# Kernel tuning notes

Hardware: AMD Instinct MI355X
Metric: run time of the kernel (lower is better)

Reference implementation:

```python
import jax, jax.numpy as jnp
import numpy as np

B, T, V, Dw, Df, H, L, F_ = 16, 96, 32000, 512, 512, 1024, 100, 64
EPS = 1e-8
SOS = 0


def setup_inputs() -> dict:
    key = jax.random.key(0)
    ks = jax.random.split(key, 24)
    rn = lambda k, s, sc=0.02: (jax.random.normal(k, s) * sc).astype(jnp.float32)
    pos_mask = (jax.random.uniform(ks[1], (B, F_, L)) < 0.3).astype(jnp.float32)
    pos_mask = jnp.maximum(pos_mask, jax.nn.one_hot(jnp.zeros((B, F_), jnp.int32), L))
    return {
        "fact_embeddings": rn(ks[0], (B, F_, Df), 1.0),
        "pos_mask": pos_mask,
        "emb": rn(ks[2], (V, Dw), 0.05),
        "W_ih": rn(ks[3], (4 * H, Df + Dw + L)),
        "W_hh": rn(ks[4], (4 * H, H)),
        "b_ih": jnp.zeros(4 * H, jnp.float32),
        "b_hh": jnp.zeros(4 * H, jnp.float32),
        "Wf1": rn(ks[5], (H, H + Df)), "bf1": jnp.zeros(H, jnp.float32),
        "Wf2": rn(ks[6], (Df, H)), "bf2": jnp.zeros(Df, jnp.float32),
        "Wc1": rn(ks[7], (H, H + Df)), "bc1": jnp.zeros(H, jnp.float32),
        "Wc2": rn(ks[8], (1, H)), "bc2": jnp.zeros(1, jnp.float32),
        "Wv1": rn(ks[9], (H, H + Df)), "bv1": jnp.zeros(H, jnp.float32),
        "Wv2": rn(ks[10], (Dw, H)), "bv2": jnp.zeros(Dw, jnp.float32),
        "Wp1": rn(ks[11], (H, H + Df)), "bp1": jnp.zeros(H, jnp.float32),
        "Wp2": rn(ks[12], (100, H)), "bp2": jnp.zeros(100, jnp.float32),
        "WP": rn(ks[13], (L, 100)), "bP": jnp.zeros(L, jnp.float32),
        "true_w": jax.random.randint(ks[14], (B, T), 0, L),
        "true_a": jax.random.randint(ks[15], (B, T), 0, F_),
        "true_z": jax.random.randint(ks[16], (B, T), 0, 2),
        "num_facts": jax.random.randint(ks[17], (B,), 1, F_),
    }


def reference(fact_embeddings, pos_mask, emb, W_ih, W_hh, b_ih, b_hh,
              Wf1, bf1, Wf2, bf2, Wc1, bc1, Wc2, bc2,
              Wv1, bv1, Wv2, bv2, Wp1, bp1, Wp2, bp2, WP, bP,
              true_w, true_a, true_z, num_facts):
    def mlp(x, W1, b1, W2, b2):
        return W2 @ jax.nn.relu(W1 @ x + b1) + b2

    def single(fe, pmask_b, tw, ta, tz, nf):
        # fe: [F_, Df]  pmask_b: [F_, L]  tw/ta/tz: [T]
        idx = jnp.arange(F_)
        valid = (idx < nf).astype(jnp.float32)
        attn_mask = jnp.where(idx == F_ - 1, 1.0, valid)  # NaF slot always allowed
        e_k = (fe * valid[:, None]).sum(0) / nf.astype(jnp.float32)

        def step(carry, inputs):
            a_prev, h, c, wv, wo = carry
            w_t, a_true, z_true = inputs
            x = jnp.concatenate([a_prev, wv, wo])  # [Df+Dw+L]
            gates = W_ih @ x + b_ih + W_hh @ h + b_hh
            i_g, f_g, g_g, o_g = jnp.split(gates, 4)
            c = jax.nn.sigmoid(f_g) * c + jax.nn.sigmoid(i_g) * jnp.tanh(g_g)
            h = jax.nn.sigmoid(o_g) * jnp.tanh(c)
            oe = jnp.concatenate([h, e_k])
            k_fact = mlp(oe, Wf1, bf1, Wf2, bf2)           # [Df]
            prob_a = jax.nn.softmax(fe @ k_fact)           # [F_]
            m = attn_mask * prob_a + EPS
            m = m / m.sum()
            log_m = jnp.log(m)
            a_idx = jnp.argmax(m)
            a_vec = fe[a_idx]
            oa = jnp.concatenate([h, a_vec])
            z = jax.nn.sigmoid(mlp(oa, Wc1, bc1, Wc2, bc2))[0]
            k_voca = mlp(oa, Wv1, bv1, Wv2, bv2)           # [Dw]
            log_w = jax.nn.log_softmax(emb @ k_voca)       # [V]
            k_pos = mlp(oa, Wp1, bp1, Wp2, bp2)            # [100]
            prob_pos = jax.nn.softmax(WP @ k_pos + bP)     # [L]
            mp = pmask_b[a_true] * prob_pos + EPS
            mp = mp / mp.sum()
            log_pos = jnp.log(mp)
            zf = z_true.astype(jnp.float32)
            loss = (-log_m[a_true]
                    + jnp.where(z_true == 0, -log_w[w_t], -log_pos[w_t])
                    - (zf * jnp.log(z) + (1.0 - zf) * jnp.log(1.0 - z)))
            wv_next = jnp.where(z_true == 0, emb[w_t], jnp.zeros(Dw, jnp.float32))
            wo_next = jnp.where(z_true == 0, jnp.zeros(L, jnp.float32), jax.nn.one_hot(w_t, L))
            return (a_vec, h, c, wv_next, wo_next), loss

        carry0 = (jnp.zeros(Df, jnp.float32), jnp.zeros(H, jnp.float32),
                  jnp.zeros(H, jnp.float32), emb[SOS], jnp.zeros(L, jnp.float32))
        _, losses = jax.lax.scan(step, carry0, (tw, ta, tz))
        return losses.sum()

    return jax.vmap(single)(fact_embeddings, pos_mask, true_w, true_a, true_z, num_facts).sum()
```

## Files before the change

kernel.cpp:

```cpp
#include <hip/hip_runtime.h>
#include <math.h>

#define TT 96
#define VV 32000
#define EPSF 1e-8f

typedef __attribute__((ext_vector_type(8))) short short8;
typedef __attribute__((ext_vector_type(4))) float f4v;

__device__ __forceinline__ float wsum64(float v){
  #pragma unroll
  for (int m=32;m>0;m>>=1) v += __shfl_xor(v,m);
  return v;
}
__device__ __forceinline__ float sigm(float x){ return 1.0f/(1.0f+expf(-x)); }
__device__ __forceinline__ float softplus(float x){ return x>20.0f ? x : log1pf(expf(x)); }
__device__ __forceinline__ float bf2f(unsigned short u){ return __uint_as_float(((unsigned)u)<<16); }
__device__ __forceinline__ unsigned short f2bf(float f){
  unsigned u = __float_as_uint(f);
  return (unsigned short)((u + 0x7fffu + ((u>>16)&1u)) >> 16);
}

__device__ __forceinline__ void core_chunk(
  const float4* __restrict__ w0, const float4* __restrict__ w1,
  const float4* __restrict__ w2, const float4* __restrict__ w3,
  const float4* __restrict__ xl, int l, int g, float (&acc)[4][4])
{
  #pragma unroll
  for (int kt=0; kt<8; kt++){
    int i = kt*16 + l;
    float4 a0=w0[i], a1=w1[i], a2=w2[i], a3=w3[i];
    #pragma unroll
    for (int j=0;j<4;j++){
      float4 x = xl[(4*g+j)*129 + i];
      acc[0][j] += a0.x*x.x + a0.y*x.y + a0.z*x.z + a0.w*x.w;
      acc[1][j] += a1.x*x.x + a1.y*x.y + a1.z*x.z + a1.w*x.w;
      acc[2][j] += a2.x*x.x + a2.y*x.y + a2.z*x.z + a2.w*x.w;
      acc[3][j] += a3.x*x.x + a3.y*x.y + a3.z*x.z + a3.w*x.w;
    }
  }
}

__device__ __forceinline__ float reduce_pick(float (&acc)[4][4], int l){
  float r = 0.f;
  #pragma unroll
  for (int ri=0;ri<4;ri++)
  #pragma unroll
  for (int j=0;j<4;j++){
    float v = acc[ri][j];
    v += __shfl_xor(v,1); v += __shfl_xor(v,2);
    v += __shfl_xor(v,4); v += __shfl_xor(v,8);
    if (l == ri*4+j) r = v;
  }
  return r;
}


__global__ __launch_bounds__(256) void k_step1(
  const float* __restrict__ Whh, float* __restrict__ hall,
  const float* __restrict__ Pw, const float* __restrict__ Pa,
  const int* __restrict__ aall, float* __restrict__ c, int t)
{
  __shared__ float4 xl[16*129];
  __shared__ float sg[256];
  int tid = threadIdx.x, lane = tid & 63, wave = tid >> 6;
  int l = lane & 15, g = lane >> 4;
  int j0 = blockIdx.x*4;
  const float4* h4 = (const float4*)hall + (size_t)t*4096;
  float acc[4][4] = {};
  for (int kc=0; kc<2; kc++){
    for (int idx=tid; idx<2048; idx+=256){
      int b = idx>>7, i = idx&127;
      xl[b*129+i] = h4[b*256 + kc*128 + i];
    }
    __syncthreads();
    const float4* w0 = (const float4*)(Whh + (size_t)(wave*1024 + j0+0)*1024) + kc*128;
    const float4* w1 = (const float4*)(Whh + (size_t)(wave*1024 + j0+1)*1024) + kc*128;
    const float4* w2 = (const float4*)(Whh + (size_t)(wave*1024 + j0+2)*1024) + kc*128;
    const float4* w3 = (const float4*)(Whh + (size_t)(wave*1024 + j0+3)*1024) + kc*128;
    core_chunk(w0,w1,w2,w3, xl, l, g, acc);
    __syncthreads();
  }
  float v = reduce_pick(acc, l);
  int r = l>>2;
  int b = g*4 + (l&3);
  int row = wave*1024 + j0 + r;
  float e = Pw[((size_t)(b*96+t))*4096 + row];
  if (t > 0){
    int ai = aall[(t-1)*16 + b];
    e += Pa[((size_t)(b*64+ai))*4096 + row];
  }
  sg[wave*64 + r*16 + b] = v + e;
  __syncthreads();
  if (tid < 64){
    int jj = j0 + (tid>>4), bb = tid&15;
    float ig = sg[  0 + (tid>>4)*16 + bb];
    float fg = sg[ 64 + (tid>>4)*16 + bb];
    float gg = sg[128 + (tid>>4)*16 + bb];
    float og = sg[192 + (tid>>4)*16 + bb];
    int ci = bb*1024 + jj;
    float cn = sigm(fg)*c[ci] + sigm(ig)*tanhf(gg);
    c[ci] = cn;
    hall[((size_t)(t+1)*16 + bb)*1024 + jj] = sigm(og)*tanhf(cn);
  }
}

__global__ __launch_bounds__(256) void k_tf(
  const float* __restrict__ Wf1, const float* __restrict__ hall,
  const float* __restrict__ cf, float* __restrict__ tf, int t)
{
  __shared__ float4 xl[16*129];
  int tid = threadIdx.x, lane = tid & 63, wave = tid >> 6;
  int l = lane & 15, g = lane >> 4;
  int rl0 = blockIdx.x*16 + wave*4;
  const float4* h4 = (const float4*)hall + (size_t)(t+1)*4096;
  float acc[4][4] = {};
  for (int kc=0; kc<2; kc++){
    for (int idx=tid; idx<2048; idx+=256){
      int b = idx>>7, i = idx&127;
      xl[b*129+i] = h4[b*256 + kc*128 + i];
    }
    __syncthreads();
    const float4* w0 = (const float4*)(Wf1 + (size_t)(rl0+0)*1536) + kc*128;
    const float4* w1 = (const float4*)(Wf1 + (size_t)(rl0+1)*1536) + kc*128;
    const float4* w2 = (const float4*)(Wf1 + (size_t)(rl0+2)*1536) + kc*128;
    const float4* w3 = (const float4*)(Wf1 + (size_t)(rl0+3)*1536) + kc*128;
    core_chunk(w0,w1,w2,w3, xl, l, g, acc);
    __syncthreads();
  }
  float v = reduce_pick(acc, l);
  int rl = rl0 + (l>>2);
  int b = g*4 + (l&3);
  tf[b*1024 + rl] = fmaxf(v + cf[b*1024 + rl], 0.f);
}

__global__ __launch_bounds__(256) void k_fk(
  const float* __restrict__ Wf2, const float* __restrict__ bf2,
  const float* __restrict__ tf, float* __restrict__ kfact)
{
  __shared__ float4 xl[16*129];
  int tid = threadIdx.x, lane = tid & 63, wave = tid >> 6;
  int l = lane & 15, g = lane >> 4;
  int row0 = blockIdx.x*16 + wave*4;
  const float4* X4 = (const float4*)tf;
  float acc[4][4] = {};
  for (int kc=0; kc<2; kc++){
    for (int idx=tid; idx<2048; idx+=256){
      int b = idx>>7, i = idx&127;
      xl[b*129+i] = X4[b*256 + kc*128 + i];
    }
    __syncthreads();
    const float4* w0 = (const float4*)(Wf2 + (size_t)(row0+0)*1024) + kc*128;
    const float4* w1 = (const float4*)(Wf2 + (size_t)(row0+1)*1024) + kc*128;
    const float4* w2 = (const float4*)(Wf2 + (size_t)(row0+2)*1024) + kc*128;
    const float4* w3 = (const float4*)(Wf2 + (size_t)(row0+3)*1024) + kc*128;
    core_chunk(w0,w1,w2,w3, xl, l, g, acc);
    __syncthreads();
  }
  float v = reduce_pick(acc, l);
  int row = row0 + (l>>2);
  int b = g*4 + (l&3);
  kfact[b*512 + row] = v + bf2[row];
}

__global__ __launch_bounds__(256) void k_attn(
  const float* __restrict__ fe, const float* __restrict__ kfact,
  const int* __restrict__ ta, const int* __restrict__ nfp,
  int* __restrict__ aall, float* __restrict__ loss, int t)
{
  __shared__ float sS[64];
  int b = blockIdx.x, tid = threadIdx.x;
  int f = tid >> 2, q = tid & 3;
  const float4* fe4 = (const float4*)(fe + ((size_t)b*64 + f)*512);
  const float4* kf4 = (const float4*)(kfact + b*512);
  float acc = 0.f;
  for (int j=0;j<32;j++){
    int i = q*32 + j;
    float4 a = fe4[i], k = kf4[i];
    acc += a.x*k.x + a.y*k.y + a.z*k.z + a.w*k.w;
  }
  acc += __shfl_xor(acc,1);
  acc += __shfl_xor(acc,2);
  if (q==0) sS[f] = acc;
  __syncthreads();
  if (tid < 64){
    int nf = nfp[b];
    float s = sS[tid];
    float mx = s;
    #pragma unroll
    for (int m=32;m>0;m>>=1) mx = fmaxf(mx, __shfl_xor(mx,m));
    float p = expf(s - mx);
    float ps = wsum64(p);
    p /= ps;
    bool mask = (tid < nf) || (tid == 63);
    float mval = mask ? (p + EPSF) : EPSF;
    float msum = wsum64(mval);
    float bv = mval; int bi2 = tid;
    #pragma unroll
    for (int m=32;m>0;m>>=1){
      float ov = __shfl_xor(bv,m); int oi = __shfl_xor(bi2,m);
      if (ov > bv || (ov == bv && oi < bi2)){ bv = ov; bi2 = oi; }
    }
    int at = ta[b*TT + t];
    float mat = __shfl(mval, at);
    if (tid == 0){
      atomicAdd(loss, -(logf(mat) - logf(msum)));
      aall[t*16 + b] = bi2;
    }
  }
}


__global__ __launch_bounds__(256) void k2_cvp(
  const float* __restrict__ Wc1, const float* __restrict__ Wv1,
  const float* __restrict__ Wp1, const float* __restrict__ hall,
  const float* __restrict__ Ph, const int* __restrict__ aall,
  const float* __restrict__ bc1, const float* __restrict__ bv1,
  const float* __restrict__ bp1, float* __restrict__ tcvp)
{
  __shared__ float4 xl[16*129];
  int tid = threadIdx.x, lane = tid & 63, wave = tid >> 6;
  int l = lane & 15, g = lane >> 4;
  int seg = blockIdx.x >> 6;
  int rl0 = (blockIdx.x & 63)*16 + wave*4;
  const float* W = (seg==0)?Wc1:(seg==1)?Wv1:Wp1;
  const float4* h4 = (const float4*)hall + (size_t)(16 + blockIdx.y*16)*256;
  float acc[4][4] = {};
  for (int kc=0; kc<2; kc++){
    for (int idx=tid; idx<2048; idx+=256){
      int cc = idx>>7, i = idx&127;
      xl[cc*129+i] = h4[cc*256 + kc*128 + i];
    }
    __syncthreads();
    const float4* w0 = (const float4*)(W + (size_t)(rl0+0)*1536) + kc*128;
    const float4* w1 = (const float4*)(W + (size_t)(rl0+1)*1536) + kc*128;
    const float4* w2 = (const float4*)(W + (size_t)(rl0+2)*1536) + kc*128;
    const float4* w3 = (const float4*)(W + (size_t)(rl0+3)*1536) + kc*128;
    core_chunk(w0,w1,w2,w3, xl, l, g, acc);
    __syncthreads();
  }
  float v = reduce_pick(acc, l);
  int rl = rl0 + (l>>2);
  int n = blockIdx.y*16 + g*4 + (l&3);
  int b = n & 15;
  int ai = aall[n];
  const float* bias = (seg==0)?bc1:(seg==1)?bv1:bp1;
  float vv = v + Ph[((size_t)(b*64+ai))*3072 + seg*1024 + rl] + bias[rl];
  tcvp[(size_t)n*3072 + seg*1024 + rl] = fmaxf(vv, 0.f);
}

__global__ __launch_bounds__(256) void k2_heads2(
  const float* __restrict__ Wv2, const float* __restrict__ bv2,
  const float* __restrict__ Wp2, const float* __restrict__ bp2,
  const float* __restrict__ Wc2, const float* __restrict__ bc2,
  const float* __restrict__ tcvp, unsigned short* __restrict__ kvh,
  float* __restrict__ kpall, float* __restrict__ zlall)
{
  __shared__ float4 xl[16*129];
  int tid = threadIdx.x, lane = tid & 63, wave = tid >> 6;
  int l = lane & 15, g = lane >> 4;
  int bx = blockIdx.x;
  int seg = (bx < 32) ? 0 : (bx < 39) ? 1 : 2;
  int rb  = (seg==0) ? bx*16 : (seg==1) ? (bx-32)*16 : 0;
  int rl0 = rb + wave*4;
  const float* WS = (seg==0)?Wv2:(seg==1)?Wp2:Wc2;
  int maxr = (seg==0)?511:(seg==1)?99:0;
  int xoff4 = (seg==0)?256:(seg==1)?512:0;
  const float4* X4 = (const float4*)tcvp;
  float acc[4][4] = {};
  for (int kc=0; kc<2; kc++){
    for (int idx=tid; idx<2048; idx+=256){
      int cc = idx>>7, i = idx&127;
      xl[cc*129+i] = X4[(size_t)(blockIdx.y*16+cc)*768 + xoff4 + kc*128 + i];
    }
    __syncthreads();
    const float4* w0 = (const float4*)(WS + (size_t)min(rl0+0,maxr)*1024) + kc*128;
    const float4* w1 = (const float4*)(WS + (size_t)min(rl0+1,maxr)*1024) + kc*128;
    const float4* w2 = (const float4*)(WS + (size_t)min(rl0+2,maxr)*1024) + kc*128;
    const float4* w3 = (const float4*)(WS + (size_t)min(rl0+3,maxr)*1024) + kc*128;
    core_chunk(w0,w1,w2,w3, xl, l, g, acc);
    __syncthreads();
  }
  float v = reduce_pick(acc, l);
  int rl = rl0 + (l>>2);
  int n = blockIdx.y*16 + g*4 + (l&3);
  if (seg==0) kvh[(size_t)n*512 + rl] = f2bf(v + bv2[rl]);
  else if (seg==1){ if (rl < 100) kpall[n*128 + rl] = v + bp2[rl]; }
  else { if (rl == 0) zlall[n] = v + bc2[0]; }
}

__global__ __launch_bounds__(256) void k2_vocab(
  const unsigned short* __restrict__ embh, const unsigned short* __restrict__ kvh,
  float2* __restrict__ part)
{
  int wid = blockIdx.x*4 + (threadIdx.x>>6);
  int lane = threadIdx.x & 63;
  int mtile = wid % 500, ntile = wid / 500;
  int mrow = mtile*64 + (lane&15);
  int ncol = ntile*64 + (lane&15);
  int ko = (lane>>4)*8;
  f4v acc[4][4];
  #pragma unroll
  for (int i=0;i<4;i++)
  #pragma unroll
  for (int j=0;j<4;j++)
  #pragma unroll
  for (int r=0;r<4;r++) acc[i][j][r] = 0.f;
  for (int kk=0; kk<512; kk+=32){
    short8 af[4], bfr[4];
    #pragma unroll
    for (int i=0;i<4;i++)
      af[i] = *(const short8*)(embh + (size_t)(mrow+16*i)*512 + kk + ko);
    #pragma unroll
    for (int i=0;i<4;i++)
      bfr[i] = *(const short8*)(kvh + (size_t)(ncol+16*i)*512 + kk + ko);
    #pragma unroll
    for (int i=0;i<4;i++)
      #pragma unroll
      for (int j=0;j<4;j++)
        acc[i][j] = __builtin_amdgcn_mfma_f32_16x16x32_bf16(af[i], bfr[j], acc[i][j], 0,0,0);
  }
  int q = lane>>4;
  #pragma unroll
  for (int j=0;j<4;j++){
    float mx = -3.4e38f;
    #pragma unroll
    for (int i=0;i<4;i++)
    #pragma unroll
    for (int r=0;r<4;r++) mx = fmaxf(mx, acc[i][j][r]);
    mx = fmaxf(mx, __shfl_xor(mx,16));
    mx = fmaxf(mx, __shfl_xor(mx,32));
    float s = 0.f;
    #pragma unroll
    for (int i=0;i<4;i++)
    #pragma unroll
    for (int r=0;r<4;r++) s += expf(acc[i][j][r] - mx);
    s += __shfl_xor(s,16);
    s += __shfl_xor(s,32);
    if (q==0){
      int col = ntile*64 + 16*j + (lane&15);
      part[(size_t)col*500 + mtile] = make_float2(mx, s);
    }
  }
}

__global__ __launch_bounds__(256) void k2_vfin(
  const float2* __restrict__ part, const unsigned short* __restrict__ embh,
  const unsigned short* __restrict__ kvh, const int* __restrict__ tw,
  const int* __restrict__ tz, float* __restrict__ loss)
{
  __shared__ float red[4];
  int n = blockIdx.x, tid = threadIdx.x;
  int t = n>>4, b = n&15;
  float mx = -3.4e38f;
  for (int i=tid; i<500; i+=256) mx = fmaxf(mx, part[(size_t)n*500+i].x);
  #pragma unroll
  for (int m=32;m>0;m>>=1) mx = fmaxf(mx, __shfl_xor(mx,m));
  if ((tid&63)==0) red[tid>>6] = mx;
  __syncthreads();
  float M = fmaxf(fmaxf(red[0],red[1]), fmaxf(red[2],red[3]));
  __syncthreads();
  float s = 0.f;
  for (int i=tid; i<500; i+=256){
    float2 p = part[(size_t)n*500+i];
    s += p.y * expf(p.x - M);
  }
  s = wsum64(s);
  if ((tid&63)==0) red[tid>>6] = s;
  __syncthreads();
  float S = red[0]+red[1]+red[2]+red[3];
  __syncthreads();
  int w = tw[b*96+t];
  float d = 0.f;
  {
    const unsigned short* er = embh + (size_t)w*512;
    const unsigned short* kr = kvh + (size_t)n*512;
    for (int i=tid; i<512; i+=256) d += bf2f(er[i])*bf2f(kr[i]);
  }
  d = wsum64(d);
  if ((tid&63)==0) red[tid>>6] = d;
  __syncthreads();
  if (tid==0 && tz[b*96+t]==0){
    float D = red[0]+red[1]+red[2]+red[3];
    atomicAdd(loss, -(D - (M + logf(S))));
  }
}

__global__ __launch_bounds__(128) void k2_posz(
  const float* __restrict__ kpall, const float* __restrict__ zlall,
  const float* __restrict__ WP, const float* __restrict__ bP,
  const float* __restrict__ pmask, const int* __restrict__ tw,
  const int* __restrict__ ta, const int* __restrict__ tz,
  float* __restrict__ loss)
{
  __shared__ float pp[100];
  int n = blockIdx.x, tid = threadIdx.x;
  int t = n>>4, b = n&15;
  if (tid < 100){
    float s = bP[tid];
    const float* wr = WP + tid*100;
    const float* kp = kpall + n*128;
    for (int j=0;j<100;j++) s += wr[j]*kp[j];
    pp[tid] = s;
  }
  __syncthreads();
  if (tid == 0){
    float u = zlall[n];
    int z = tz[b*96+t], w = tw[b*96+t], at = ta[b*96+t];
    float tot = z ? softplus(-u) : softplus(u);
    if (z){
      float mxv = -1e30f;
      for (int l2=0;l2<100;l2++) mxv = fmaxf(mxv, pp[l2]);
      float se = 0.f;
      for (int l2=0;l2<100;l2++) se += expf(pp[l2]-mxv);
      const float* pm = pmask + ((size_t)b*64 + at)*100;
      float msum = 0.f, mw = 0.f;
      for (int l2=0;l2<100;l2++){
        float m = pm[l2]*(expf(pp[l2]-mxv)/se) + EPSF;
        msum += m;
        if (l2==w) mw = m;
      }
      tot += -(logf(mw) - logf(msum));
    }
    atomicAdd(loss, tot);
  }
}


__global__ void k_cvt_emb(const float* __restrict__ emb, unsigned* __restrict__ out){
  const int n = VV*512/2;
  for (int idx = blockIdx.x*256 + threadIdx.x; idx < n; idx += gridDim.x*256){
    float2 v = ((const float2*)emb)[idx];
    unsigned a = __float_as_uint(v.x), b = __float_as_uint(v.y);
    unsigned ra = (a + 0x7fffu + ((a>>16)&1u)) >> 16;
    unsigned rb = (b + 0x7fffu + ((b>>16)&1u)) >> 16;
    out[idx] = ra | (rb<<16);
  }
}

__global__ void k_setup(const float* __restrict__ fe, const int* __restrict__ nfp,
                        float* __restrict__ e_k){
  int b = blockIdx.x, tid = threadIdx.x;
  int nf = nfp[b];
  for (int d=tid; d<512; d+=256){
    float s = 0.f;
    for (int f=0; f<nf; f++) s += fe[((size_t)b*64+f)*512 + d];
    e_k[b*512+d] = s/(float)nf;
  }
}

__global__ __launch_bounds__(256) void k_pre_pa(
  const float* __restrict__ Wih, const float* __restrict__ fe, float* __restrict__ Pa)
{
  __shared__ float4 xl[16*129];
  int tid = threadIdx.x, lane = tid & 63, wave = tid >> 6;
  int l = lane & 15, g = lane >> 4;
  int row0 = blockIdx.x*16 + wave*4;
  int c0 = blockIdx.y*16;
  const float4* fe4 = (const float4*)fe;
  for (int idx=tid; idx<2048; idx+=256){
    int cc = idx>>7, i = idx&127;
    xl[cc*129+i] = fe4[(size_t)(c0+cc)*128 + i];
  }
  __syncthreads();
  const float4* w0 = (const float4*)(Wih + (size_t)(row0+0)*1124);
  const float4* w1 = (const float4*)(Wih + (size_t)(row0+1)*1124);
  const float4* w2 = (const float4*)(Wih + (size_t)(row0+2)*1124);
  const float4* w3 = (const float4*)(Wih + (size_t)(row0+3)*1124);
  float acc[4][4] = {};
  core_chunk(w0,w1,w2,w3, xl, l, g, acc);
  float v = reduce_pick(acc, l);
  int row = row0 + (l>>2), c = c0 + g*4 + (l&3);
  Pa[(size_t)c*4096 + row] = v;
}

__global__ __launch_bounds__(256) void k_pre_ph(
  const float* __restrict__ Wc1, const float* __restrict__ Wv1,
  const float* __restrict__ Wp1, const float* __restrict__ fe, float* __restrict__ Ph)
{
  __shared__ float4 xl[16*129];
  int tid = threadIdx.x, lane = tid & 63, wave = tid >> 6;
  int l = lane & 15, g = lane >> 4;
  int row0 = blockIdx.x*16 + wave*4;
  int head = row0 >> 10, rl0 = row0 & 1023;
  const float* W = (head==0)?Wc1:(head==1)?Wv1:Wp1;
  int c0 = blockIdx.y*16;
  const float4* fe4 = (const float4*)fe;
  for (int idx=tid; idx<2048; idx+=256){
    int cc = idx>>7, i = idx&127;
    xl[cc*129+i] = fe4[(size_t)(c0+cc)*128 + i];
  }
  __syncthreads();
  const float4* w0 = (const float4*)(W + (size_t)(rl0+0)*1536 + 1024);
  const float4* w1 = (const float4*)(W + (size_t)(rl0+1)*1536 + 1024);
  const float4* w2 = (const float4*)(W + (size_t)(rl0+2)*1536 + 1024);
  const float4* w3 = (const float4*)(W + (size_t)(rl0+3)*1536 + 1024);
  float acc[4][4] = {};
  core_chunk(w0,w1,w2,w3, xl, l, g, acc);
  float v = reduce_pick(acc, l);
  int row = row0 + (l>>2), c = c0 + g*4 + (l&3);
  Ph[(size_t)c*3072 + row] = v;
}

__global__ __launch_bounds__(256) void k_pre_pw(
  const float* __restrict__ Wih, const float* __restrict__ emb,
  const int* __restrict__ tw, const int* __restrict__ tz,
  const float* __restrict__ bih, const float* __restrict__ bhh,
  float* __restrict__ Pw)
{
  __shared__ float4 xl[16*129];
  int tid = threadIdx.x, lane = tid & 63, wave = tid >> 6;
  int l = lane & 15, g = lane >> 4;
  int row0 = blockIdx.x*16 + wave*4;
  int c0 = blockIdx.y*16;
  for (int idx=tid; idx<2048; idx+=256){
    int cc = idx>>7, i = idx&127;
    int c = c0+cc, b = c/96, t2 = c - b*96;
    int w=0, z=0;
    if (t2>0){ w = tw[b*96+t2-1]; z = tz[b*96+t2-1]; }
    float4 v = make_float4(0.f,0.f,0.f,0.f);
    if (z==0) v = ((const float4*)emb)[(size_t)w*128 + i];
    xl[cc*129+i] = v;
  }
  __syncthreads();
  const float4* w0 = (const float4*)(Wih + (size_t)(row0+0)*1124 + 512);
  const float4* w1 = (const float4*)(Wih + (size_t)(row0+1)*1124 + 512);
  const float4* w2 = (const float4*)(Wih + (size_t)(row0+2)*1124 + 512);
  const float4* w3 = (const float4*)(Wih + (size_t)(row0+3)*1124 + 512);
  float acc[4][4] = {};
  core_chunk(w0,w1,w2,w3, xl, l, g, acc);
  float v = reduce_pick(acc, l);
  int row = row0 + (l>>2), c = c0 + g*4 + (l&3);
  int b = c/96, t2 = c - b*96;
  int w=0, z=0;
  if (t2>0){ w = tw[b*96+t2-1]; z = tz[b*96+t2-1]; }
  v += bih[row] + bhh[row];
  if (z) v += Wih[(size_t)row*1124 + 1024 + w];
  Pw[(size_t)c*4096 + row] = v;
}

__global__ __launch_bounds__(256) void k_pre_cf(
  const float* __restrict__ Wf1, const float* __restrict__ bf1,
  const float* __restrict__ e_k, float* __restrict__ cf)
{
  __shared__ float4 xl[16*129];
  int tid = threadIdx.x, lane = tid & 63, wave = tid >> 6;
  int l = lane & 15, g = lane >> 4;
  int row0 = blockIdx.x*16 + wave*4;
  const float4* ek4 = (const float4*)e_k;
  for (int idx=tid; idx<2048; idx+=256){
    int cc = idx>>7, i = idx&127;
    xl[cc*129+i] = ek4[cc*128 + i];
  }
  __syncthreads();
  const float4* w0 = (const float4*)(Wf1 + (size_t)(row0+0)*1536 + 1024);
  const float4* w1 = (const float4*)(Wf1 + (size_t)(row0+1)*1536 + 1024);
  const float4* w2 = (const float4*)(Wf1 + (size_t)(row0+2)*1536 + 1024);
  const float4* w3 = (const float4*)(Wf1 + (size_t)(row0+3)*1536 + 1024);
  float acc[4][4] = {};
  core_chunk(w0,w1,w2,w3, xl, l, g, acc);
  float v = reduce_pick(acc, l);
  int row = row0 + (l>>2), b = g*4 + (l&3);
  cf[b*1024 + row] = v + bf1[row];
}

__global__ void k_out(const float* __restrict__ loss, float* __restrict__ out){
  out[0] = loss[0];
}

extern "C" void kernel_launch(void* const* d_in, const int* in_sizes, int n_in,
                              void* d_out, int out_size, void* d_ws, size_t ws_size,
                              hipStream_t stream)
{
  const float* fe   = (const float*)d_in[0];
  const float* pmask= (const float*)d_in[1];
  const float* emb  = (const float*)d_in[2];
  const float* Wih  = (const float*)d_in[3];
  const float* Whh  = (const float*)d_in[4];
  const float* bih  = (const float*)d_in[5];
  const float* bhh  = (const float*)d_in[6];
  const float* Wf1  = (const float*)d_in[7];
  const float* bf1  = (const float*)d_in[8];
  const float* Wf2  = (const float*)d_in[9];
  const float* bf2  = (const float*)d_in[10];
  const float* Wc1  = (const float*)d_in[11];
  const float* bc1  = (const float*)d_in[12];
  const float* Wc2  = (const float*)d_in[13];
  const float* bc2  = (const float*)d_in[14];
  const float* Wv1  = (const float*)d_in[15];
  const float* bv1  = (const float*)d_in[16];
  const float* Wv2  = (const float*)d_in[17];
  const float* bv2  = (const float*)d_in[18];
  const float* Wp1  = (const float*)d_in[19];
  const float* bp1  = (const float*)d_in[20];
  const float* Wp2  = (const float*)d_in[21];
  const float* bp2  = (const float*)d_in[22];
  const float* WP   = (const float*)d_in[23];
  const float* bP   = (const float*)d_in[24];
  const int* tw  = (const int*)d_in[25];
  const int* ta  = (const int*)d_in[26];
  const int* tz  = (const int*)d_in[27];
  const int* nfp = (const int*)d_in[28];

  float* w = (float*)d_ws;
  float*    loss  = w + 0;
  float*    c     = w + 16;
  float*    hall  = w + 16400;
  int*      aall  = (int*)(w + 1605648);
  float*    tf    = w + 1607184;
  float*    kfact = w + 1623568;
  float*    e_k   = w + 1631760;
  float*    cf    = w + 1639952;
  float*    kpall = w + 1656336;
  float*    zlall = w + 1852944;
  float*    tcvp  = w + 1854480;
  float2*   part  = (float2*)(w + 6573072);
  unsigned short* kvh = (unsigned short*)(w + 8109072);
  float*    Pa    = w + 8502288;
  float*    Ph    = w + 12696592;
  float*    Pw    = w + 15842320;
  unsigned* embbf = (unsigned*)(w + 22133776);
  const unsigned short* embh = (const unsigned short*)embbf;

  hipMemsetAsync(d_ws, 0, (size_t)(16 + 16384 + 16384)*4, stream);
  k_cvt_emb<<<8192,256,0,stream>>>(emb, embbf);
  k_setup<<<16,256,0,stream>>>(fe, nfp, e_k);
  k_pre_pa<<<dim3(256,64),256,0,stream>>>(Wih, fe, Pa);
  k_pre_ph<<<dim3(192,64),256,0,stream>>>(Wc1, Wv1, Wp1, fe, Ph);
  k_pre_pw<<<dim3(256,96),256,0,stream>>>(Wih, emb, tw, tz, bih, bhh, Pw);
  k_pre_cf<<<64,256,0,stream>>>(Wf1, bf1, e_k, cf);

  for (int t=0; t<TT; t++){
    k_step1<<<256,256,0,stream>>>(Whh, hall, Pw, Pa, aall, c, t);
    k_tf<<<64,256,0,stream>>>(Wf1, hall, cf, tf, t);
    k_fk<<<32,256,0,stream>>>(Wf2, bf2, tf, kfact);
    k_attn<<<16,256,0,stream>>>(fe, kfact, ta, nfp, aall, loss, t);
  }

  k2_cvp<<<dim3(192,96),256,0,stream>>>(Wc1, Wv1, Wp1, hall, Ph, aall,
                                        bc1, bv1, bp1, tcvp);
  k2_heads2<<<dim3(40,96),256,0,stream>>>(Wv2, bv2, Wp2, bp2, Wc2, bc2,
                                          tcvp, kvh, kpall, zlall);
  k2_vocab<<<3000,256,0,stream>>>(embh, kvh, part);
  k2_vfin<<<1536,256,0,stream>>>(part, embh, kvh, tw, tz, loss);
  k2_posz<<<1536,128,0,stream>>>(kpall, zlall, WP, bP, pmask, tw, ta, tz, loss);
  k_out<<<1,1,0,stream>>>(loss, (float*)d_out);
}
```

Baseline: 5.350 ms.

## Fuse recurrent loop into persistent kernel with grid barriers and fold Wf2

The per-timestep launches of four small kernels are replaced by one persistent 256-block kernel. It loops over all timesteps and separates the LSTM, the fact-MLP hidden layer and the attention stages with a global atomic-counter barrier. The second fact-MLP layer is folded algebraically into a precomputed fact_embeddings·Wf2 product (Gb) plus a bias term, which removes a dependent matmul stage per step. This targets launch overhead and serial stage latency. In exchange it relies on all 256 blocks being co-resident, adds spin-wait barrier costs, and makes the attention dot products longer (1024 instead of 512).

Measured after the change: 15.34 ms. +186.7%, slower.

```diff
diff --git a/kernel.cpp b/kernel.cpp
--- a/kernel.cpp
+++ b/kernel.cpp
@@ -21,6 +21,19 @@
   return (unsigned short)((u + 0x7fffu + ((u>>16)&1u)) >> 16);
 }
 
+__device__ __forceinline__ void gbar(unsigned* cnt, unsigned target){
+  __syncthreads();
+  if (threadIdx.x == 0){
+    __threadfence();
+    __hip_atomic_fetch_add(cnt, 1u, __ATOMIC_ACQ_REL, __HIP_MEMORY_SCOPE_AGENT);
+    while (__hip_atomic_load(cnt, __ATOMIC_ACQUIRE, __HIP_MEMORY_SCOPE_AGENT) < target){
+      __builtin_amdgcn_s_sleep(1);
+    }
+    __threadfence();
+  }
+  __syncthreads();
+}
+
 __device__ __forceinline__ void core_chunk(
   const float4* __restrict__ w0, const float4* __restrict__ w1,
   const float4* __restrict__ w2, const float4* __restrict__ w3,
@@ -55,158 +68,137 @@
   return r;
 }
 
-
-__global__ __launch_bounds__(256) void k_step1(
+__global__ __launch_bounds__(256) void k_phase1(
   const float* __restrict__ Whh, float* __restrict__ hall,
   const float* __restrict__ Pw, const float* __restrict__ Pa,
-  const int* __restrict__ aall, float* __restrict__ c, int t)
+  int* __restrict__ aall, float* __restrict__ c,
+  const float* __restrict__ Wf1, const float* __restrict__ cf,
+  float* __restrict__ tf,
+  const float* __restrict__ Gb, const float* __restrict__ gb0,
+  const int* __restrict__ ta, const int* __restrict__ nfp,
+  float* __restrict__ loss, unsigned* __restrict__ bar)
 {
   __shared__ float4 xl[16*129];
   __shared__ float sg[256];
+  __shared__ float sS[64];
   int tid = threadIdx.x, lane = tid & 63, wave = tid >> 6;
   int l = lane & 15, g = lane >> 4;
-  int j0 = blockIdx.x*4;
-  const float4* h4 = (const float4*)hall + (size_t)t*4096;
-  float acc[4][4] = {};
-  for (int kc=0; kc<2; kc++){
-    for (int idx=tid; idx<2048; idx+=256){
-      int b = idx>>7, i = idx&127;
-      xl[b*129+i] = h4[b*256 + kc*128 + i];
-    }
-    __syncthreads();
-    const float4* w0 = (const float4*)(Whh + (size_t)(wave*1024 + j0+0)*1024) + kc*128;
-    const float4* w1 = (const float4*)(Whh + (size_t)(wave*1024 + j0+1)*1024) + kc*128;
-    const float4* w2 = (const float4*)(Whh + (size_t)(wave*1024 + j0+2)*1024) + kc*128;
-    const float4* w3 = (const float4*)(Whh + (size_t)(wave*1024 + j0+3)*1024) + kc*128;
-    core_chunk(w0,w1,w2,w3, xl, l, g, acc);
-    __syncthreads();
-  }
-  float v = reduce_pick(acc, l);
-  int r = l>>2;
-  int b = g*4 + (l&3);
-  int row = wave*1024 + j0 + r;
-  float e = Pw[((size_t)(b*96+t))*4096 + row];
-  if (t > 0){
-    int ai = aall[(t-1)*16 + b];
-    e += Pa[((size_t)(b*64+ai))*4096 + row];
-  }
-  sg[wave*64 + r*16 + b] = v + e;
-  __syncthreads();
-  if (tid < 64){
-    int jj = j0 + (tid>>4), bb = tid&15;
-    float ig = sg[  0 + (tid>>4)*16 + bb];
-    float fg = sg[ 64 + (tid>>4)*16 + bb];
-    float gg = sg[128 + (tid>>4)*16 + bb];
-    float og = sg[192 + (tid>>4)*16 + bb];
-    int ci = bb*1024 + jj;
-    float cn = sigm(fg)*c[ci] + sigm(ig)*tanhf(gg);
-    c[ci] = cn;
-    hall[((size_t)(t+1)*16 + bb)*1024 + jj] = sigm(og)*tanhf(cn);
-  }
-}
-
-__global__ __launch_bounds__(256) void k_tf(
-  const float* __restrict__ Wf1, const float* __restrict__ hall,
-  const float* __restrict__ cf, float* __restrict__ tf, int t)
-{
-  __shared__ float4 xl[16*129];
-  int tid = threadIdx.x, lane = tid & 63, wave = tid >> 6;
-  int l = lane & 15, g = lane >> 4;
-  int rl0 = blockIdx.x*16 + wave*4;
-  const float4* h4 = (const float4*)hall + (size_t)(t+1)*4096;
-  float acc[4][4] = {};
-  for (int kc=0; kc<2; kc++){
-    for (int idx=tid; idx<2048; idx+=256){
-      int b = idx>>7, i = idx&127;
-      xl[b*129+i] = h4[b*256 + kc*128 + i];
-    }
-    __syncthreads();
-    const float4* w0 = (const float4*)(Wf1 + (size_t)(rl0+0)*1536) + kc*128;
-    const float4* w1 = (const float4*)(Wf1 + (size_t)(rl0+1)*1536) + kc*128;
-    const float4* w2 = (const float4*)(Wf1 + (size_t)(rl0+2)*1536) + kc*128;
-    const float4* w3 = (const float4*)(Wf1 + (size_t)(rl0+3)*1536) + kc*128;
-    core_chunk(w0,w1,w2,w3, xl, l, g, acc);
-    __syncthreads();
-  }
-  float v = reduce_pick(acc, l);
-  int rl = rl0 + (l>>2);
-  int b = g*4 + (l&3);
-  tf[b*1024 + rl] = fmaxf(v + cf[b*1024 + rl], 0.f);
-}
-
-__global__ __launch_bounds__(256) void k_fk(
-  const float* __restrict__ Wf2, const float* __restrict__ bf2,
-  const float* __restrict__ tf, float* __restrict__ kfact)
-{
-  __shared__ float4 xl[16*129];
-  int tid = threadIdx.x, lane = tid & 63, wave = tid >> 6;
-  int l = lane & 15, g = lane >> 4;
-  int row0 = blockIdx.x*16 + wave*4;
-  const float4* X4 = (const float4*)tf;
-  float acc[4][4] = {};
-  for (int kc=0; kc<2; kc++){
-    for (int idx=tid; idx<2048; idx+=256){
-      int b = idx>>7, i = idx&127;
-      xl[b*129+i] = X4[b*256 + kc*128 + i];
-    }
-    __syncthreads();
-    const float4* w0 = (const float4*)(Wf2 + (size_t)(row0+0)*1024) + kc*128;
-    const float4* w1 = (const float4*)(Wf2 + (size_t)(row0+1)*1024) + kc*128;
-    const float4* w2 = (const float4*)(Wf2 + (size_t)(row0+2)*1024) + kc*128;
-    const float4* w3 = (const float4*)(Wf2 + (size_t)(row0+3)*1024) + kc*128;
-    core_chunk(w0,w1,w2,w3, xl, l, g, acc);
-    __syncthreads();
-  }
-  float v = reduce_pick(acc, l);
-  int row = row0 + (l>>2);
-  int b = g*4 + (l&3);
-  kfact[b*512 + row] = v + bf2[row];
-}
-
-__global__ __launch_bounds__(256) void k_attn(
-  const float* __restrict__ fe, const float* __restrict__ kfact,
-  const int* __restrict__ ta, const int* __restrict__ nfp,
-  int* __restrict__ aall, float* __restrict__ loss, int t)
-{
-  __shared__ float sS[64];
-  int b = blockIdx.x, tid = threadIdx.x;
-  int f = tid >> 2, q = tid & 3;
-  const float4* fe4 = (const float4*)(fe + ((size_t)b*64 + f)*512);
-  const float4* kf4 = (const float4*)(kfact + b*512);
-  float acc = 0.f;
-  for (int j=0;j<32;j++){
-    int i = q*32 + j;
-    float4 a = fe4[i], k = kf4[i];
-    acc += a.x*k.x + a.y*k.y + a.z*k.z + a.w*k.w;
-  }
-  acc += __shfl_xor(acc,1);
-  acc += __shfl_xor(acc,2);
-  if (q==0) sS[f] = acc;
-  __syncthreads();
-  if (tid < 64){
-    int nf = nfp[b];
-    float s = sS[tid];
-    float mx = s;
-    #pragma unroll
-    for (int m=32;m>0;m>>=1) mx = fmaxf(mx, __shfl_xor(mx,m));
-    float p = expf(s - mx);
-    float ps = wsum64(p);
-    p /= ps;
-    bool mask = (tid < nf) || (tid == 63);
-    float mval = mask ? (p + EPSF) : EPSF;
-    float msum = wsum64(mval);
-    float bv = mval; int bi2 = tid;
-    #pragma unroll
-    for (int m=32;m>0;m>>=1){
-      float ov = __shfl_xor(bv,m); int oi = __shfl_xor(bi2,m);
-      if (ov > bv || (ov == bv && oi < bi2)){ bv = ov; bi2 = oi; }
-    }
-    int at = ta[b*TT + t];
-    float mat = __shfl(mval, at);
-    if (tid == 0){
-      atomicAdd(loss, -(logf(mat) - logf(msum)));
-      aall[t*16 + b] = bi2;
-    }
+  int wg = blockIdx.x;
+  unsigned rnd = 0;
+
+  for (int t=0; t<TT; t++){
+    {
+      int j0 = wg*4;
+      const float4* h4 = (const float4*)hall + (size_t)t*4096;
+      float acc[4][4] = {};
+      for (int kc=0; kc<2; kc++){
+        for (int idx=tid; idx<2048; idx+=256){
+          int b = idx>>7, i = idx&127;
+          xl[b*129+i] = h4[b*256 + kc*128 + i];
+        }
+        __syncthreads();
+        const float4* w0 = (const float4*)(Whh + (size_t)(wave*1024 + j0+0)*1024) + kc*128;
+        const float4* w1 = (const float4*)(Whh + (size_t)(wave*1024 + j0+1)*1024) + kc*128;
+        const float4* w2 = (const float4*)(Whh + (size_t)(wave*1024 + j0+2)*1024) + kc*128;
+        const float4* w3 = (const float4*)(Whh + (size_t)(wave*1024 + j0+3)*1024) + kc*128;
+        core_chunk(w0,w1,w2,w3, xl, l, g, acc);
+        __syncthreads();
+      }
+      float v = reduce_pick(acc, l);
+      int r = l>>2;
+      int b = g*4 + (l&3);
+      int row = wave*1024 + j0 + r;
+      float e = Pw[((size_t)(b*96+t))*4096 + row];
+      if (t > 0){
+        int ai = aall[(t-1)*16 + b];
+        e += Pa[((size_t)(b*64+ai))*4096 + row];
+      }
+      sg[wave*64 + r*16 + b] = v + e;
+      __syncthreads();
+      if (tid < 64){
+        int jj = j0 + (tid>>4), bb = tid&15;
+        float ig = sg[  0 + (tid>>4)*16 + bb];
+        float fg = sg[ 64 + (tid>>4)*16 + bb];
+        float gg = sg[128 + (tid>>4)*16 + bb];
+        float og = sg[192 + (tid>>4)*16 + bb];
+        int ci = bb*1024 + jj;
+        float cn = sigm(fg)*c[ci] + sigm(ig)*tanhf(gg);
+        c[ci] = cn;
+        hall[((size_t)(t+1)*16 + bb)*1024 + jj] = sigm(og)*tanhf(cn);
+      }
+    }
+    rnd++; gbar(bar, rnd*256u);
+
+    if (wg < 64){
+      int rl0 = wg*16 + wave*4;
+      const float4* h4 = (const float4*)hall + (size_t)(t+1)*4096;
+      float acc[4][4] = {};
+      for (int kc=0; kc<2; kc++){
+        for (int idx=tid; idx<2048; idx+=256){
+          int b = idx>>7, i = idx&127;
+          xl[b*129+i] = h4[b*256 + kc*128 + i];
+        }
+        __syncthreads();
+        const float4* w0 = (const float4*)(Wf1 + (size_t)(rl0+0)*1536) + kc*128;
+        const float4* w1 = (const float4*)(Wf1 + (size_t)(rl0+1)*1536) + kc*128;
+        const float4* w2 = (const float4*)(Wf1 + (size_t)(rl0+2)*1536) + kc*128;
+        const float4* w3 = (const float4*)(Wf1 + (size_t)(rl0+3)*1536) + kc*128;
+        core_chunk(w0,w1,w2,w3, xl, l, g, acc);
+        __syncthreads();
+      }
+      float v = reduce_pick(acc, l);
+      int rl = rl0 + (l>>2);
+      int b = g*4 + (l&3);
+      tf[b*1024 + rl] = fmaxf(v + cf[b*1024 + rl], 0.f);
+    }
+    rnd++; gbar(bar, rnd*256u);
+
+    if (wg < 16){
+      int b = wg;
+      float* stf = (float*)xl;
+      ((float4*)stf)[tid] = ((const float4*)(tf + b*1024))[tid];
+      __syncthreads();
+      int f = tid>>2, q = tid&3;
+      const float4* G4 = (const float4*)(Gb + (size_t)(b*64+f)*1024);
+      const float4* st4 = (const float4*)stf;
+      float acc = 0.f;
+      for (int j=0;j<64;j++){
+        int i = q*64 + j;
+        float4 a = G4[i], x = st4[i];
+        acc += a.x*x.x + a.y*x.y + a.z*x.z + a.w*x.w;
+      }
+      acc += __shfl_xor(acc,1);
+      acc += __shfl_xor(acc,2);
+      if (q==0) sS[f] = acc + gb0[b*64+f];
+      __syncthreads();
+      if (tid < 64){
+        int nf = nfp[b];
+        float s = sS[tid];
+        float mx = s;
+        #pragma unroll
+        for (int m=32;m>0;m>>=1) mx = fmaxf(mx, __shfl_xor(mx,m));
+        float p = expf(s - mx);
+        float ps = wsum64(p);
+        p /= ps;
+        bool mask = (tid < nf) || (tid == 63);
+        float mval = mask ? (p + EPSF) : EPSF;
+        float msum = wsum64(mval);
+        float bv = mval; int bi2 = tid;
+        #pragma unroll
+        for (int m=32;m>0;m>>=1){
+          float ov = __shfl_xor(bv,m); int oi = __shfl_xor(bi2,m);
+          if (ov > bv || (ov == bv && oi < bi2)){ bv = ov; bi2 = oi; }
+        }
+        int at = ta[b*TT + t];
+        float mat = __shfl(mval, at);
+        if (tid == 0){
+          atomicAdd(loss, -(logf(mat) - logf(msum)));
+          aall[t*16 + b] = bi2;
+        }
+      }
+      __syncthreads();
+    }
+    rnd++; gbar(bar, rnd*256u);
   }
 }
 
@@ -562,6 +554,49 @@
   float v = reduce_pick(acc, l);
   int row = row0 + (l>>2), b = g*4 + (l&3);
   cf[b*1024 + row] = v + bf1[row];
+}
+
+__global__ __launch_bounds__(256) void k_pre_g(
+  const float* __restrict__ Wf2, const float* __restrict__ fe, float* __restrict__ Gb)
+{
+  __shared__ float fs[16][128];
+  int tid = threadIdx.x;
+  int r0 = blockIdx.x*16;
+  int k0 = blockIdx.y*256;
+  float acc[16] = {};
+  for (int dc=0; dc<4; dc++){
+    for (int idx=tid; idx<2048; idx+=256){
+      int r = idx>>7, d = idx&127;
+      fs[r][d] = fe[(size_t)(r0+r)*512 + dc*128 + d];
+    }
+    __syncthreads();
+    for (int d=0; d<128; d++){
+      float w = Wf2[(size_t)(dc*128+d)*1024 + k0 + tid];
+      #pragma unroll
+      for (int r=0;r<16;r++) acc[r] += fs[r][d]*w;
+    }
+    __syncthreads();
+  }
+  #pragma unroll
+  for (int r=0;r<16;r++) Gb[(size_t)(r0+r)*1024 + k0 + tid] = acc[r];
+}
+
+__global__ __launch_bounds__(256) void k_gb0(
+  const float* __restrict__ fe, const float* __restrict__ bf2, float* __restrict__ gb0)
+{
+  int b = blockIdx.x;
+  int f = threadIdx.x>>2, q = threadIdx.x&3;
+  const float4* fe4 = (const float4*)(fe + ((size_t)b*64+f)*512);
+  const float4* b4 = (const float4*)bf2;
+  float acc = 0.f;
+  for (int j=0;j<32;j++){
+    int i = q*32+j;
+    float4 a = fe4[i], x = b4[i];
+    acc += a.x*x.x + a.y*x.y + a.z*x.z + a.w*x.w;
+  }
+  acc += __shfl_xor(acc,1);
+  acc += __shfl_xor(acc,2);
+  if (q==0) gb0[b*64+f] = acc;
 }
 
 __global__ void k_out(const float* __restrict__ loss, float* __restrict__ out){
@@ -604,16 +639,18 @@
 
   float* w = (float*)d_ws;
   float*    loss  = w + 0;
+  unsigned* bar   = (unsigned*)(w + 8);
   float*    c     = w + 16;
   float*    hall  = w + 16400;
   int*      aall  = (int*)(w + 1605648);
   float*    tf    = w + 1607184;
-  float*    kfact = w + 1623568;
+  float*    gb0   = w + 1623568;
   float*    e_k   = w + 1631760;
   float*    cf    = w + 1639952;
   float*    kpall = w + 1656336;
   float*    zlall = w + 1852944;
   float*    tcvp  = w + 1854480;
+  float*    Gb    = w + 1854480;
   float2*   part  = (float2*)(w + 6573072);
   unsigned short* kvh = (unsigned short*)(w + 8109072);
   float*    Pa    = w + 8502288;
@@ -629,13 +666,11 @@
   k_pre_ph<<<dim3(192,64),256,0,stream>>>(Wc1, Wv1, Wp1, fe, Ph);
   k_pre_pw<<<dim3(256,96),256,0,stream>>>(Wih, emb, tw, tz, bih, bhh, Pw);
   k_pre_cf<<<64,256,0,stream>>>(Wf1, bf1, e_k, cf);
-
-  for (int t=0; t<TT; t++){
-    k_step1<<<256,256,0,stream>>>(Whh, hall, Pw, Pa, aall, c, t);
-    k_tf<<<64,256,0,stream>>>(Wf1, hall, cf, tf, t);
-    k_fk<<<32,256,0,stream>>>(Wf2, bf2, tf, kfact);
-    k_attn<<<16,256,0,stream>>>(fe, kfact, ta, nfp, aall, loss, t);
-  }
+  k_pre_g<<<dim3(64,4),256,0,stream>>>(Wf2, fe, Gb);
+  k_gb0<<<16,256,0,stream>>>(fe, bf2, gb0);
+
+  k_phase1<<<256,256,0,stream>>>(Whh, hall, Pw, Pa, aall, c, Wf1, cf, tf,
+                                 Gb, gb0, ta, nfp, loss, bar);
 
   k2_cvp<<<dim3(192,96),256,0,stream>>>(Wc1, Wv1, Wp1, hall, Ph, aall,
                                         bc1, bv1, bp1, tcvp);
```
